# Kernel optimization log

Measured on AMD Instinct MI355X. Metric: run time of the kernel, lower is better.

## Reference

```python
import jax, jax.numpy as jnp
import numpy as np

N, C, H, G, VOCAB = 1024, 1, 512, 16, 32000


def setup_inputs() -> dict:
    key = jax.random.key(0)
    ks = jax.random.split(key, 8)
    x = jax.random.randint(ks[0], (C,), 0, VOCAB)
    z = jax.random.randint(ks[1], (N, C), 0, G)
    h = jax.random.normal(ks[2], (N, C, H), dtype=jnp.float32)
    E = jax.random.normal(ks[3], (VOCAB, H), dtype=jnp.float32) * 0.02
    W = jax.random.normal(ks[4], (G, H, H), dtype=jnp.float32) * 0.05
    U = jax.random.normal(ks[5], (G, H, H), dtype=jnp.float32) * 0.05
    Vw = jax.random.normal(ks[6], (VOCAB, H), dtype=jnp.float32) * 0.02
    Vb = jax.random.normal(ks[7], (VOCAB,), dtype=jnp.float32) * 0.01
    return {"x": x, "z": z, "h": h, "E": E, "W": W, "U": U, "Vw": Vw, "Vb": Vb}


def reference(x, z, h, E, W, U, Vw, Vb):
    # e: (C,H) token embeddings shared across batch (matches torch 'ch' subscript)
    e = E[x]
    # Class-indexed weight gather: W[z], U[z] have shape (N,C,H,H)
    Wz = W[z]
    Uz = U[z]
    # h_t[n,c,k] = tanh( sum_h Wz[n,c,k,h]*e[c,h] + sum_h Uz[n,c,k,h]*h[n,c,h] )
    h_t = jnp.tanh(jnp.einsum('nckh,ch->nck', Wz, e)
                   + jnp.einsum('nckh,nch->nck', Uz, h))
    # Output projection V: (N,C,H) @ (H,VOCAB) + bias
    logits = jnp.einsum('nck,vk->ncv', h_t, Vw) + Vb
    return (logits, h_t)
```

## Files before the change

### kernel.cpp

```cpp
#include <hip/hip_runtime.h>
#include <hip/hip_bf16.h>


#define N_ROWS  1024
#define H_DIM   512
#define N_GRP   16
#define VOCAB_N 32000

typedef __attribute__((ext_vector_type(4))) float    f32x4;
typedef __attribute__((ext_vector_type(8))) short    short8;
typedef __attribute__((ext_vector_type(8))) __bf16   bf16x8;
typedef __attribute__((ext_vector_type(2))) _Float16 half2;
typedef __attribute__((ext_vector_type(4))) _Float16 half4;
typedef __attribute__((ext_vector_type(8))) _Float16 half8;

__device__ __forceinline__ unsigned short f2bf(float f) {
  unsigned int u = __builtin_bit_cast(unsigned int, f);
  return (unsigned short)((u + 0x7FFFu + ((u >> 16) & 1u)) >> 16);
}

__device__ __forceinline__ float fdot2f(half2 a, half2 b, float c) {
#if defined(__has_builtin)
#if __has_builtin(__builtin_amdgcn_fdot2)
  return __builtin_amdgcn_fdot2(a, b, c, false);
#else
  return c + (float)a.x * (float)b.x + (float)a.y * (float)b.y;
#endif
#else
  return c + (float)a.x * (float)b.x + (float)a.y * (float)b.y;
#endif
}

__device__ __forceinline__ f32x4 MFMA16(short8 a, short8 b, f32x4 c) {
  return __builtin_amdgcn_mfma_f32_16x16x32_bf16(
      __builtin_bit_cast(bf16x8, a), __builtin_bit_cast(bf16x8, b), c, 0, 0, 0);
}

__global__ void k_sort(const int* __restrict__ z, int* __restrict__ perm,
                       int* __restrict__ offs) {
  __shared__ int cnt[N_GRP], pos[N_GRP];
  const int t = threadIdx.x;
  if (t < N_GRP) cnt[t] = 0;
  __syncthreads();
  const int g = z[t];
  atomicAdd(&cnt[g], 1);
  __syncthreads();
  if (t == 0) {
    int acc = 0;
    for (int i = 0; i < N_GRP; ++i) { pos[i] = acc; offs[i] = acc; acc += cnt[i]; }
    offs[N_GRP] = acc;
  }
  __syncthreads();
  const int p = atomicAdd(&pos[g], 1);
  perm[p] = t;
}

__global__ void k_we(const int* __restrict__ x, const float* __restrict__ E,
                     const float* __restrict__ W, float* __restrict__ We) {
  const int gid  = blockIdx.x * blockDim.x + threadIdx.x;
  const int wv   = gid >> 6;
  const int lane = threadIdx.x & 63;
  const f32x4* e4 = (const f32x4*)(E + (size_t)x[0] * H_DIM);
  const f32x4* w4 = (const f32x4*)(W + (size_t)wv * H_DIM);
  f32x4 a0 = w4[lane],      b0 = e4[lane];
  f32x4 a1 = w4[lane + 64], b1 = e4[lane + 64];
  float acc = a0.x * b0.x + a0.y * b0.y + a0.z * b0.z + a0.w * b0.w
            + a1.x * b1.x + a1.y * b1.y + a1.z * b1.z + a1.w * b1.w;
#pragma unroll
  for (int o = 32; o; o >>= 1) acc += __shfl_down(acc, o);
  if (lane == 0) We[wv] = acc;
}

__global__ __launch_bounds__(256, 1)
void k_ht(const float* __restrict__ h, const float* __restrict__ U,
          const float* __restrict__ We, const int* __restrict__ perm,
          const int* __restrict__ offs, float* __restrict__ ht_out,
          unsigned short* __restrict__ A) {
  __shared__ __align__(16) _Float16 Us[64][520];
  __shared__ __align__(16) _Float16 Hs[64][520];
  __shared__ int rowidx[64];

  const int bid = blockIdx.x;
  const int g   = bid & 15;
  const int kt  = (bid >> 4) & 7;
  const int rh  = bid >> 7;
  const int off = offs[g];
  const int cn  = offs[g + 1] - off;
  if (cn <= 0) return;
  const int hcnt = (cn + 1) >> 1;
  const int r0 = rh * hcnt;
  const int r1 = min(cn, r0 + hcnt);
  if (r0 >= r1) return;

  const int tid = threadIdx.x;
  const int k0  = kt * 64;

  {
    const f32x4* src = (const f32x4*)(U + ((size_t)g * H_DIM + k0) * H_DIM);
    for (int idx = tid; idx < 64 * 128; idx += 256) {
      const int k = idx >> 7, h4 = idx & 127;
      f32x4 v = src[(size_t)k * 128 + h4];
      half4 hv;
      hv.x = (_Float16)v.x; hv.y = (_Float16)v.y;
      hv.z = (_Float16)v.z; hv.w = (_Float16)v.w;
      *(half4*)&Us[k][h4 * 4] = hv;
    }
  }

  const int kq = tid & 15;
  const int rq = tid >> 4;
  float we[4];
#pragma unroll
  for (int a = 0; a < 4; ++a) we[a] = We[g * H_DIM + k0 + kq + 16 * a];

  for (int p = r0; p < r1; p += 64) {
    __syncthreads();
    if (tid < 64) rowidx[tid] = (p + tid < r1) ? perm[off + p + tid] : -1;
    __syncthreads();
    for (int idx = tid; idx < 64 * 128; idx += 256) {
      const int i = idx >> 7, h4 = idx & 127;
      const int row = rowidx[i];
      if (row >= 0) {
        f32x4 v = *(const f32x4*)(h + (size_t)row * H_DIM + h4 * 4);
        half4 hv;
        hv.x = (_Float16)v.x; hv.y = (_Float16)v.y;
        hv.z = (_Float16)v.z; hv.w = (_Float16)v.w;
        *(half4*)&Hs[i][h4 * 4] = hv;
      }
    }
    __syncthreads();

    int ib[4]; bool vb[4];
#pragma unroll
    for (int b = 0; b < 4; ++b) { ib[b] = rq + 16 * b; vb[b] = (p + rq + 16 * b < r1); }
    float acc[4][4];
#pragma unroll
    for (int a = 0; a < 4; ++a)
#pragma unroll
      for (int b = 0; b < 4; ++b) acc[a][b] = we[a];

    for (int hh = 0; hh < H_DIM; hh += 8) {
      half8 u[4], hv[4];
#pragma unroll
      for (int a = 0; a < 4; ++a) u[a] = *(const half8*)&Us[kq + 16 * a][hh];
#pragma unroll
      for (int b = 0; b < 4; ++b) if (vb[b]) hv[b] = *(const half8*)&Hs[ib[b]][hh];
#pragma unroll
      for (int a = 0; a < 4; ++a)
#pragma unroll
        for (int b = 0; b < 4; ++b) {
          if (vb[b]) {
#pragma unroll
            for (int t = 0; t < 4; ++t) {
              half2 ua; ua.x = u[a][2 * t];  ua.y = u[a][2 * t + 1];
              half2 hb; hb.x = hv[b][2 * t]; hb.y = hv[b][2 * t + 1];
              acc[a][b] = fdot2f(ua, hb, acc[a][b]);
            }
          }
        }
    }

#pragma unroll
    for (int b = 0; b < 4; ++b) {
      if (vb[b]) {
        const int row = rowidx[ib[b]];
#pragma unroll
        for (int a = 0; a < 4; ++a) {
          const int k = k0 + kq + 16 * a;
          const float val = tanhf(acc[a][b]);
          ht_out[(size_t)row * H_DIM + k] = val;
          A[(size_t)row * H_DIM + k]     = f2bf(val);
        }
      }
    }
  }
}

__global__ __launch_bounds__(256, 1)
void k_logits(const unsigned short* __restrict__ A, const float* __restrict__ Vw,
              const float* __restrict__ Vb, float* __restrict__ out) {
  __shared__ __align__(16) unsigned short Bs[64 * 512];
  __shared__ __align__(16) unsigned short As[2][256 * 64];

  const int tid  = threadIdx.x;
  const int wid  = tid >> 6;
  const int lane = tid & 63;
  const int lr   = lane & 15;
  const int lk   = lane >> 4;
  const int v0   = blockIdx.x * 64;

  for (int idx = tid; idx < 64 * 64; idx += 256) {
    const int v  = idx >> 6;
    const int k8 = idx & 63;
    const float* s = Vw + (size_t)(v0 + v) * H_DIM + k8 * 8;
    f32x4 x0 = *(const f32x4*)s;
    f32x4 x1 = *(const f32x4*)(s + 4);
    short8 b;
    b[0] = (short)f2bf(x0.x); b[1] = (short)f2bf(x0.y);
    b[2] = (short)f2bf(x0.z); b[3] = (short)f2bf(x0.w);
    b[4] = (short)f2bf(x1.x); b[5] = (short)f2bf(x1.y);
    b[6] = (short)f2bf(x1.z); b[7] = (short)f2bf(x1.w);
    const int byt = v * 1024 + ((k8 * 16) ^ ((v & 7) << 4));
    *(short8*)((char*)Bs + byt) = b;
  }

  float vbr[4];
#pragma unroll
  for (int fn = 0; fn < 4; ++fn) vbr[fn] = Vb[v0 + fn * 16 + lr];

  short8 stg[8];
#pragma unroll
  for (int j = 0; j < 8; ++j) {
    const int c = j * 256 + tid;
    const int r = c >> 3, c16 = c & 7;
    stg[j] = *(const short8*)(A + (size_t)r * H_DIM + c16 * 8);
  }
#pragma unroll
  for (int j = 0; j < 8; ++j) {
    const int c = j * 256 + tid;
    const int r = c >> 3, c16 = c & 7;
    *(short8*)((char*)As[0] + r * 128 + ((c16 * 16) ^ ((r & 7) << 4))) = stg[j];
  }
  __syncthreads();

  f32x4 acc[4][4];
  for (int step = 0; step < 32; ++step) {
    const int mi = step >> 3, kb = step & 7, cur = step & 1;
    if (kb == 0) {
#pragma unroll
      for (int a = 0; a < 4; ++a)
#pragma unroll
        for (int b = 0; b < 4; ++b) acc[a][b] = f32x4{0.f, 0.f, 0.f, 0.f};
    }
    if (step < 31) {
      const int ns = step + 1, nmi = ns >> 3, nkb = ns & 7;
#pragma unroll
      for (int j = 0; j < 8; ++j) {
        const int c = j * 256 + tid;
        const int r = c >> 3, c16 = c & 7;
        stg[j] = *(const short8*)(A + (size_t)(nmi * 256 + r) * H_DIM + nkb * 64 + c16 * 8);
      }
    }
#pragma unroll
    for (int ks = 0; ks < 2; ++ks) {
      short8 af[4], bfrag[4];
      const int abyt = (ks * 32 + lk * 8) * 2;
      const int kbyt = (kb * 64 + ks * 32 + lk * 8) * 2;
#pragma unroll
      for (int fm = 0; fm < 4; ++fm) {
        const int r = wid * 64 + fm * 16 + lr;
        af[fm] = *(const short8*)((const char*)As[cur] + r * 128 + (abyt ^ ((r & 7) << 4)));
      }
#pragma unroll
      for (int fn = 0; fn < 4; ++fn) {
        const int v = fn * 16 + lr;
        bfrag[fn] = *(const short8*)((const char*)Bs + v * 1024 + (kbyt ^ ((v & 7) << 4)));
      }
#pragma unroll
      for (int fm = 0; fm < 4; ++fm)
#pragma unroll
        for (int fn = 0; fn < 4; ++fn)
          acc[fm][fn] = MFMA16(af[fm], bfrag[fn], acc[fm][fn]);
    }
    if (step < 31) {
      const int nb = cur ^ 1;
#pragma unroll
      for (int j = 0; j < 8; ++j) {
        const int c = j * 256 + tid;
        const int r = c >> 3, c16 = c & 7;
        *(short8*)((char*)As[nb] + r * 128 + ((c16 * 16) ^ ((r & 7) << 4))) = stg[j];
      }
    }
    __syncthreads();
    if (kb == 7) {
      const int m0 = mi * 256;
#pragma unroll
      for (int fm = 0; fm < 4; ++fm) {
        const int row = m0 + wid * 64 + fm * 16 + lk * 4;
#pragma unroll
        for (int fn = 0; fn < 4; ++fn) {
          const int col = v0 + fn * 16 + lr;
          float* o = out + (size_t)row * VOCAB_N + col;
#pragma unroll
          for (int r = 0; r < 4; ++r)
            o[(size_t)r * VOCAB_N] = acc[fm][fn][r] + vbr[fn];
        }
      }
    }
  }
}

extern "C" void kernel_launch(void* const* d_in, const int* in_sizes, int n_in,
                              void* d_out, int out_size, void* d_ws, size_t ws_size,
                              hipStream_t stream) {
  const int*   x  = (const int*)d_in[0];
  const int*   z  = (const int*)d_in[1];
  const float* h  = (const float*)d_in[2];
  const float* E  = (const float*)d_in[3];
  const float* W  = (const float*)d_in[4];
  const float* U  = (const float*)d_in[5];
  const float* Vw = (const float*)d_in[6];
  const float* Vb = (const float*)d_in[7];

  float* logits = (float*)d_out;
  float* ht_out = logits + (size_t)N_ROWS * VOCAB_N;

  unsigned short* wsA = (unsigned short*)d_ws;
  float* We = (float*)((char*)d_ws + (1 << 20));
  int* perm = (int*)((char*)d_ws + (1 << 20) + 32768);
  int* offs = perm + N_ROWS;

  k_sort<<<1, N_ROWS, 0, stream>>>(z, perm, offs);
  k_we<<<2048, 256, 0, stream>>>(x, E, W, We);
  k_ht<<<256, 256, 0, stream>>>(h, U, We, perm, offs, ht_out, wsA);
  k_logits<<<500, 256, 0, stream>>>(wsA, Vw, Vb, logits);
}
```

Measured before the change: 362.1 us.

## Use bf16 MFMA for h_t grouped GEMM and stream A directly in logits

The grouped recurrent projection moves from fp16 dot2 scalar accumulation to bf16 MFMA tiles. Each block now covers 64 output columns of one group, with U staged swizzled in LDS and h rows read straight from global and converted per fragment. The logits kernel drops its double-buffered LDS staging of A and reads A fragments directly from global (L2-resident), with each wave handling 256 rows. Launch bounds allow two blocks per CU. This adds bf16 rounding to the h_t path and depends on cache hits for the unstaged global reads.

```diff
diff --git a/kernel.cpp b/kernel.cpp
--- a/kernel.cpp
+++ b/kernel.cpp
@@ -10,25 +10,19 @@
 typedef __attribute__((ext_vector_type(4))) float    f32x4;
 typedef __attribute__((ext_vector_type(8))) short    short8;
 typedef __attribute__((ext_vector_type(8))) __bf16   bf16x8;
-typedef __attribute__((ext_vector_type(2))) _Float16 half2;
-typedef __attribute__((ext_vector_type(4))) _Float16 half4;
-typedef __attribute__((ext_vector_type(8))) _Float16 half8;
 
 __device__ __forceinline__ unsigned short f2bf(float f) {
   unsigned int u = __builtin_bit_cast(unsigned int, f);
   return (unsigned short)((u + 0x7FFFu + ((u >> 16) & 1u)) >> 16);
 }
 
-__device__ __forceinline__ float fdot2f(half2 a, half2 b, float c) {
-#if defined(__has_builtin)
-#if __has_builtin(__builtin_amdgcn_fdot2)
-  return __builtin_amdgcn_fdot2(a, b, c, false);
-#else
-  return c + (float)a.x * (float)b.x + (float)a.y * (float)b.y;
-#endif
-#else
-  return c + (float)a.x * (float)b.x + (float)a.y * (float)b.y;
-#endif
+__device__ __forceinline__ short8 cvt8(f32x4 x0, f32x4 x1) {
+  short8 b;
+  b[0] = (short)f2bf(x0.x); b[1] = (short)f2bf(x0.y);
+  b[2] = (short)f2bf(x0.z); b[3] = (short)f2bf(x0.w);
+  b[4] = (short)f2bf(x1.x); b[5] = (short)f2bf(x1.y);
+  b[6] = (short)f2bf(x1.z); b[7] = (short)f2bf(x1.w);
+  return b;
 }
 
 __device__ __forceinline__ f32x4 MFMA16(short8 a, short8 b, f32x4 c) {
@@ -71,116 +65,103 @@
   if (lane == 0) We[wv] = acc;
 }
 
-__global__ __launch_bounds__(256, 1)
+__global__ __launch_bounds__(256, 2)
 void k_ht(const float* __restrict__ h, const float* __restrict__ U,
           const float* __restrict__ We, const int* __restrict__ perm,
           const int* __restrict__ offs, float* __restrict__ ht_out,
           unsigned short* __restrict__ A) {
-  __shared__ __align__(16) _Float16 Us[64][520];
-  __shared__ __align__(16) _Float16 Hs[64][520];
-  __shared__ int rowidx[64];
+  __shared__ __align__(16) unsigned short Us[64 * 512];
+  __shared__ int rowidx[128];
 
   const int bid = blockIdx.x;
   const int g   = bid & 15;
-  const int kt  = (bid >> 4) & 7;
-  const int rh  = bid >> 7;
+  const int nt  = bid >> 4;
   const int off = offs[g];
   const int cn  = offs[g + 1] - off;
   if (cn <= 0) return;
-  const int hcnt = (cn + 1) >> 1;
-  const int r0 = rh * hcnt;
-  const int r1 = min(cn, r0 + hcnt);
-  if (r0 >= r1) return;
-
-  const int tid = threadIdx.x;
-  const int k0  = kt * 64;
-
-  {
-    const f32x4* src = (const f32x4*)(U + ((size_t)g * H_DIM + k0) * H_DIM);
-    for (int idx = tid; idx < 64 * 128; idx += 256) {
-      const int k = idx >> 7, h4 = idx & 127;
-      f32x4 v = src[(size_t)k * 128 + h4];
-      half4 hv;
-      hv.x = (_Float16)v.x; hv.y = (_Float16)v.y;
-      hv.z = (_Float16)v.z; hv.w = (_Float16)v.w;
-      *(half4*)&Us[k][h4 * 4] = hv;
-    }
-  }
-
-  const int kq = tid & 15;
-  const int rq = tid >> 4;
-  float we[4];
-#pragma unroll
-  for (int a = 0; a < 4; ++a) we[a] = We[g * H_DIM + k0 + kq + 16 * a];
-
-  for (int p = r0; p < r1; p += 64) {
+
+  const int tid  = threadIdx.x;
+  const int wid  = tid >> 6;
+  const int lane = tid & 63;
+  const int lr   = lane & 15;
+  const int lk   = lane >> 4;
+  const int n0   = nt * 64;
+
+  const float* ub = U + ((size_t)g * H_DIM + n0) * H_DIM;
+  for (int idx = tid; idx < 64 * 64; idx += 256) {
+    const int nn = idx >> 6, k8 = idx & 63;
+    const float* s = ub + (size_t)nn * H_DIM + k8 * 8;
+    f32x4 x0 = *(const f32x4*)s;
+    f32x4 x1 = *(const f32x4*)(s + 4);
+    *(short8*)((char*)Us + nn * 1024 + ((k8 * 16) ^ ((nn & 7) << 4))) = cvt8(x0, x1);
+  }
+
+  float wer[4];
+#pragma unroll
+  for (int fn = 0; fn < 4; ++fn) wer[fn] = We[g * H_DIM + n0 + fn * 16 + lr];
+  const int row0 = perm[off];
+
+  for (int p = 0; p < cn; p += 128) {
     __syncthreads();
-    if (tid < 64) rowidx[tid] = (p + tid < r1) ? perm[off + p + tid] : -1;
+    if (tid < 128) rowidx[tid] = (p + tid < cn) ? perm[off + p + tid] : -1;
     __syncthreads();
-    for (int idx = tid; idx < 64 * 128; idx += 256) {
-      const int i = idx >> 7, h4 = idx & 127;
-      const int row = rowidx[i];
-      if (row >= 0) {
-        f32x4 v = *(const f32x4*)(h + (size_t)row * H_DIM + h4 * 4);
-        half4 hv;
-        hv.x = (_Float16)v.x; hv.y = (_Float16)v.y;
-        hv.z = (_Float16)v.z; hv.w = (_Float16)v.w;
-        *(half4*)&Hs[i][h4 * 4] = hv;
-      }
-    }
-    __syncthreads();
-
-    int ib[4]; bool vb[4];
-#pragma unroll
-    for (int b = 0; b < 4; ++b) { ib[b] = rq + 16 * b; vb[b] = (p + rq + 16 * b < r1); }
-    float acc[4][4];
-#pragma unroll
-    for (int a = 0; a < 4; ++a)
-#pragma unroll
-      for (int b = 0; b < 4; ++b) acc[a][b] = we[a];
-
-    for (int hh = 0; hh < H_DIM; hh += 8) {
-      half8 u[4], hv[4];
-#pragma unroll
-      for (int a = 0; a < 4; ++a) u[a] = *(const half8*)&Us[kq + 16 * a][hh];
-#pragma unroll
-      for (int b = 0; b < 4; ++b) if (vb[b]) hv[b] = *(const half8*)&Hs[ib[b]][hh];
-#pragma unroll
-      for (int a = 0; a < 4; ++a)
-#pragma unroll
-        for (int b = 0; b < 4; ++b) {
-          if (vb[b]) {
-#pragma unroll
-            for (int t = 0; t < 4; ++t) {
-              half2 ua; ua.x = u[a][2 * t];  ua.y = u[a][2 * t + 1];
-              half2 hb; hb.x = hv[b][2 * t]; hb.y = hv[b][2 * t + 1];
-              acc[a][b] = fdot2f(ua, hb, acc[a][b]);
-            }
+
+    int ra[2];
+#pragma unroll
+    for (int fm = 0; fm < 2; ++fm) {
+      const int rr = rowidx[wid * 32 + fm * 16 + lr];
+      ra[fm] = (rr >= 0) ? rr : row0;
+    }
+
+    f32x4 acc[2][4];
+#pragma unroll
+    for (int fm = 0; fm < 2; ++fm)
+#pragma unroll
+      for (int fn = 0; fn < 4; ++fn) acc[fm][fn] = f32x4{0.f, 0.f, 0.f, 0.f};
+
+#pragma unroll 4
+    for (int kf = 0; kf < 16; ++kf) {
+      short8 a[2], b[4];
+#pragma unroll
+      for (int fm = 0; fm < 2; ++fm) {
+        const float* s = h + (size_t)ra[fm] * H_DIM + kf * 32 + lk * 8;
+        a[fm] = cvt8(*(const f32x4*)s, *(const f32x4*)(s + 4));
+      }
+#pragma unroll
+      for (int fn = 0; fn < 4; ++fn) {
+        const int v = fn * 16 + lr;
+        b[fn] = *(const short8*)((const char*)Us + v * 1024 +
+                                 ((kf * 64 + lk * 16) ^ ((v & 7) << 4)));
+      }
+#pragma unroll
+      for (int fm = 0; fm < 2; ++fm)
+#pragma unroll
+        for (int fn = 0; fn < 4; ++fn)
+          acc[fm][fn] = MFMA16(a[fm], b[fn], acc[fm][fn]);
+    }
+
+#pragma unroll
+    for (int fm = 0; fm < 2; ++fm)
+#pragma unroll
+      for (int r = 0; r < 4; ++r) {
+        const int row = rowidx[wid * 32 + fm * 16 + lk * 4 + r];
+        if (row >= 0) {
+#pragma unroll
+          for (int fn = 0; fn < 4; ++fn) {
+            const int n = n0 + fn * 16 + lr;
+            const float val = tanhf(acc[fm][fn][r] + wer[fn]);
+            ht_out[(size_t)row * H_DIM + n] = val;
+            A[(size_t)row * H_DIM + n]     = f2bf(val);
           }
         }
-    }
-
-#pragma unroll
-    for (int b = 0; b < 4; ++b) {
-      if (vb[b]) {
-        const int row = rowidx[ib[b]];
-#pragma unroll
-        for (int a = 0; a < 4; ++a) {
-          const int k = k0 + kq + 16 * a;
-          const float val = tanhf(acc[a][b]);
-          ht_out[(size_t)row * H_DIM + k] = val;
-          A[(size_t)row * H_DIM + k]     = f2bf(val);
-        }
-      }
-    }
-  }
-}
-
-__global__ __launch_bounds__(256, 1)
+      }
+  }
+}
+
+__global__ __launch_bounds__(256, 2)
 void k_logits(const unsigned short* __restrict__ A, const float* __restrict__ Vw,
               const float* __restrict__ Vb, float* __restrict__ out) {
   __shared__ __align__(16) unsigned short Bs[64 * 512];
-  __shared__ __align__(16) unsigned short As[2][256 * 64];
 
   const int tid  = threadIdx.x;
   const int wid  = tid >> 6;
@@ -195,96 +176,51 @@
     const float* s = Vw + (size_t)(v0 + v) * H_DIM + k8 * 8;
     f32x4 x0 = *(const f32x4*)s;
     f32x4 x1 = *(const f32x4*)(s + 4);
-    short8 b;
-    b[0] = (short)f2bf(x0.x); b[1] = (short)f2bf(x0.y);
-    b[2] = (short)f2bf(x0.z); b[3] = (short)f2bf(x0.w);
-    b[4] = (short)f2bf(x1.x); b[5] = (short)f2bf(x1.y);
-    b[6] = (short)f2bf(x1.z); b[7] = (short)f2bf(x1.w);
-    const int byt = v * 1024 + ((k8 * 16) ^ ((v & 7) << 4));
-    *(short8*)((char*)Bs + byt) = b;
+    *(short8*)((char*)Bs + v * 1024 + ((k8 * 16) ^ ((v & 7) << 4))) = cvt8(x0, x1);
   }
 
   float vbr[4];
 #pragma unroll
   for (int fn = 0; fn < 4; ++fn) vbr[fn] = Vb[v0 + fn * 16 + lr];
-
-  short8 stg[8];
-#pragma unroll
-  for (int j = 0; j < 8; ++j) {
-    const int c = j * 256 + tid;
-    const int r = c >> 3, c16 = c & 7;
-    stg[j] = *(const short8*)(A + (size_t)r * H_DIM + c16 * 8);
-  }
-#pragma unroll
-  for (int j = 0; j < 8; ++j) {
-    const int c = j * 256 + tid;
-    const int r = c >> 3, c16 = c & 7;
-    *(short8*)((char*)As[0] + r * 128 + ((c16 * 16) ^ ((r & 7) << 4))) = stg[j];
-  }
-  __syncthreads();
-
-  f32x4 acc[4][4];
-  for (int step = 0; step < 32; ++step) {
-    const int mi = step >> 3, kb = step & 7, cur = step & 1;
-    if (kb == 0) {
-#pragma unroll
-      for (int a = 0; a < 4; ++a)
-#pragma unroll
-        for (int b = 0; b < 4; ++b) acc[a][b] = f32x4{0.f, 0.f, 0.f, 0.f};
-    }
-    if (step < 31) {
-      const int ns = step + 1, nmi = ns >> 3, nkb = ns & 7;
-#pragma unroll
-      for (int j = 0; j < 8; ++j) {
-        const int c = j * 256 + tid;
-        const int r = c >> 3, c16 = c & 7;
-        stg[j] = *(const short8*)(A + (size_t)(nmi * 256 + r) * H_DIM + nkb * 64 + c16 * 8);
-      }
-    }
-#pragma unroll
-    for (int ks = 0; ks < 2; ++ks) {
-      short8 af[4], bfrag[4];
-      const int abyt = (ks * 32 + lk * 8) * 2;
-      const int kbyt = (kb * 64 + ks * 32 + lk * 8) * 2;
-#pragma unroll
-      for (int fm = 0; fm < 4; ++fm) {
-        const int r = wid * 64 + fm * 16 + lr;
-        af[fm] = *(const short8*)((const char*)As[cur] + r * 128 + (abyt ^ ((r & 7) << 4)));
-      }
+  __syncthreads();
+
+  for (int mt = 0; mt < 4; ++mt) {
+    const int m0 = wid * 256 + mt * 64;
+    f32x4 acc[4][4];
+#pragma unroll
+    for (int fm = 0; fm < 4; ++fm)
+#pragma unroll
+      for (int fn = 0; fn < 4; ++fn) acc[fm][fn] = f32x4{0.f, 0.f, 0.f, 0.f};
+
+#pragma unroll 4
+    for (int kf = 0; kf < 16; ++kf) {
+      short8 a[4], b[4];
+#pragma unroll
+      for (int fm = 0; fm < 4; ++fm)
+        a[fm] = *(const short8*)(A + (size_t)(m0 + fm * 16 + lr) * H_DIM +
+                                 kf * 32 + lk * 8);
 #pragma unroll
       for (int fn = 0; fn < 4; ++fn) {
         const int v = fn * 16 + lr;
-        bfrag[fn] = *(const short8*)((const char*)Bs + v * 1024 + (kbyt ^ ((v & 7) << 4)));
+        b[fn] = *(const short8*)((const char*)Bs + v * 1024 +
+                                 ((kf * 64 + lk * 16) ^ ((v & 7) << 4)));
       }
 #pragma unroll
       for (int fm = 0; fm < 4; ++fm)
 #pragma unroll
         for (int fn = 0; fn < 4; ++fn)
-          acc[fm][fn] = MFMA16(af[fm], bfrag[fn], acc[fm][fn]);
-    }
-    if (step < 31) {
-      const int nb = cur ^ 1;
-#pragma unroll
-      for (int j = 0; j < 8; ++j) {
-        const int c = j * 256 + tid;
-        const int r = c >> 3, c16 = c & 7;
-        *(short8*)((char*)As[nb] + r * 128 + ((c16 * 16) ^ ((r & 7) << 4))) = stg[j];
-      }
-    }
-    __syncthreads();
-    if (kb == 7) {
-      const int m0 = mi * 256;
-#pragma unroll
-      for (int fm = 0; fm < 4; ++fm) {
-        const int row = m0 + wid * 64 + fm * 16 + lk * 4;
-#pragma unroll
-        for (int fn = 0; fn < 4; ++fn) {
-          const int col = v0 + fn * 16 + lr;
-          float* o = out + (size_t)row * VOCAB_N + col;
-#pragma unroll
-          for (int r = 0; r < 4; ++r)
-            o[(size_t)r * VOCAB_N] = acc[fm][fn][r] + vbr[fn];
-        }
+          acc[fm][fn] = MFMA16(a[fm], b[fn], acc[fm][fn]);
+    }
+
+#pragma unroll
+    for (int fm = 0; fm < 4; ++fm) {
+#pragma unroll
+      for (int r = 0; r < 4; ++r) {
+        const int row = m0 + fm * 16 + lk * 4 + r;
+        float* o = out + (size_t)row * VOCAB_N + v0 + lr;
+#pragma unroll
+        for (int fn = 0; fn < 4; ++fn)
+          o[fn * 16] = acc[fm][fn][r] + vbr[fn];
       }
     }
   }
@@ -312,6 +248,6 @@
 
   k_sort<<<1, N_ROWS, 0, stream>>>(z, perm, offs);
   k_we<<<2048, 256, 0, stream>>>(x, E, W, We);
-  k_ht<<<256, 256, 0, stream>>>(h, U, We, perm, offs, ht_out, wsA);
+  k_ht<<<128, 256, 0, stream>>>(h, U, We, perm, offs, ht_out, wsA);
   k_logits<<<500, 256, 0, stream>>>(wsA, Vw, Vb, logits);
 }
```

Measured after the change: 315.2 us. -13.0%, faster.
